# Performance work log

Measured on AMD Instinct MI355X. Metric: run time of the kernel, lower is better.

The kernel has to match this reference:

```python
import jax, jax.numpy as jnp
import numpy as np

NUM_HEADS = 16
PROJECT_DIM = 1024
HEAD_DIM = PROJECT_DIM // NUM_HEADS  # 64; used only for the softmax scale


def setup_inputs() -> dict:
    key = jax.random.key(0)
    k1, k2, k3 = jax.random.split(key, 3)
    B, N, D = 8, 3072, PROJECT_DIM
    inputs = jax.random.normal(k1, (B, N, D), dtype=jnp.float32)
    wqkv = jax.random.normal(k2, (D, 3 * D), dtype=jnp.float32) * (1.0 / np.sqrt(D))
    dense_w = jax.random.normal(k3, (3 * D, D), dtype=jnp.float32) * (1.0 / np.sqrt(3 * D))
    dense_b = jnp.zeros((D,), dtype=jnp.float32)
    return {"inputs": inputs, "wqkv": wqkv, "dense_w": dense_w, "dense_b": dense_b}


def reference(inputs, wqkv, dense_w, dense_b):
    B, N, D = inputs.shape
    H = NUM_HEADS
    # fused QKV projection: [B, N, 3D]
    qkv = jnp.einsum('bnd,de->bne', inputs, wqkv)
    # separate heads: [B, H, N, 3*head_dim]
    qkv = qkv.reshape(B, N, H, (3 * D) // H).transpose(0, 2, 1, 3)
    # NOTE: faithful to source — split along TOKEN axis (axis=2) into 3 chunks
    q, k, v = jnp.split(qkv, 3, axis=2)  # each [B, H, N//3, 3*head_dim]
    scale = 1.0 / jnp.sqrt(jnp.float32(HEAD_DIM))
    logits = jnp.einsum('bhqc,bhkc->bhqk', q, k) * scale  # [B, H, N//3, N//3]
    attn = jax.nn.softmax(logits, axis=-1)
    out = jnp.einsum('bhqk,bhkc->bhqc', attn, v)  # [B, H, N//3, 3*head_dim]
    # recombine heads -> [B, N//3, 3D]
    out = out.transpose(0, 2, 1, 3).reshape(B, N // 3, 3 * D)
    # output projection -> [B, N//3, D]
    return jnp.einsum('bnc,cd->bnd', out, dense_w) + dense_b
```

## Files before the change

kernel.cpp:

```cpp
#include <hip/hip_runtime.h>
#include <hip/hip_bf16.h>

typedef unsigned short u16;
using f32x4  = __attribute__((ext_vector_type(4))) float;
using bf16x8 = __attribute__((ext_vector_type(8))) short;

typedef __attribute__((address_space(1))) const void global_cvoid;
typedef __attribute__((address_space(3))) void lds_void;

__device__ __forceinline__ void async16(const u16* g, u16* l) {
    __builtin_amdgcn_global_load_lds((global_cvoid*)g, (lds_void*)l, 16, 0, 0);
}

__device__ __forceinline__ u16 f2bf(float f) {
    union { float f; unsigned u; } cv; cv.f = f;
    unsigned r = cv.u + 0x7fff + ((cv.u >> 16) & 1);
    return (u16)(r >> 16);
}

__device__ __forceinline__ u16 f2bf_rz(float f) {
    union { float f; unsigned u; } cv; cv.f = f;
    return (u16)(cv.u >> 16);
}

__device__ __forceinline__ float dppmax16(float x) {
    union { float f; int i; } c, o;
    c.f = x;
    o.i = __builtin_amdgcn_update_dpp(0, c.i, 0xB1,  0xF, 0xF, true); c.f = fmaxf(c.f, o.f);
    o.i = __builtin_amdgcn_update_dpp(0, c.i, 0x4E,  0xF, 0xF, true); c.f = fmaxf(c.f, o.f);
    o.i = __builtin_amdgcn_update_dpp(0, c.i, 0x141, 0xF, 0xF, true); c.f = fmaxf(c.f, o.f);
    o.i = __builtin_amdgcn_update_dpp(0, c.i, 0x140, 0xF, 0xF, true); c.f = fmaxf(c.f, o.f);
    return c.f;
}
__device__ __forceinline__ float dppsum16(float x) {
    union { float f; int i; } c, o;
    c.f = x;
    o.i = __builtin_amdgcn_update_dpp(0, c.i, 0xB1,  0xF, 0xF, true); c.f += o.f;
    o.i = __builtin_amdgcn_update_dpp(0, c.i, 0x4E,  0xF, 0xF, true); c.f += o.f;
    o.i = __builtin_amdgcn_update_dpp(0, c.i, 0x141, 0xF, 0xF, true); c.f += o.f;
    o.i = __builtin_amdgcn_update_dpp(0, c.i, 0x140, 0xF, 0xF, true); c.f += o.f;
    return c.f;
}

__global__ __launch_bounds__(256) void cast_kernel(const float* __restrict__ src,
                                                   u16* __restrict__ dst, int n4) {
    int i = blockIdx.x * blockDim.x + threadIdx.x;
    int st = gridDim.x * blockDim.x;
    for (; i < n4; i += st) {
        float4 v = ((const float4*)src)[i];
        ushort4 o;
        o.x = f2bf(v.x); o.y = f2bf(v.y); o.z = f2bf(v.z); o.w = f2bf(v.w);
        ((ushort4*)dst)[i] = o;
    }
}

__global__ __launch_bounds__(256) void wtrans_kernel(const float* __restrict__ src,
                                                     u16* __restrict__ dst, int R, int C) {
    __shared__ float tile[64][68];
    int ct = blockIdx.x, rt = blockIdx.y;
    int t = threadIdx.x;
    int r = t >> 2;
    const float* s = src + (size_t)(rt * 64 + r) * C + ct * 64;
#pragma unroll
    for (int jj = 0; jj < 4; ++jj) {
        int c4 = (t & 3) + jj * 4;
        float4 v = *(const float4*)(s + c4 * 4);
        *(float4*)&tile[r][c4 * 4] = v;
    }
    __syncthreads();
    int od = t >> 2;
    u16* d = dst + (size_t)(ct * 64 + od) * R + rt * 64;
#pragma unroll
    for (int jj = 0; jj < 4; ++jj) {
        int c4 = (t & 3) + jj * 4;
        ushort4 v;
        v.x = f2bf(tile[c4 * 4 + 0][od]);
        v.y = f2bf(tile[c4 * 4 + 1][od]);
        v.z = f2bf(tile[c4 * 4 + 2][od]);
        v.w = f2bf(tile[c4 * 4 + 3][od]);
        *(ushort4*)(d + c4 * 4) = v;
    }
}

template<bool OUT_F32>
__global__ __launch_bounds__(256, 2)
void gemm_bt_kernel(const u16* __restrict__ A, const u16* __restrict__ BT,
                    void* __restrict__ Cout, const float* __restrict__ bias,
                    u16* __restrict__ VTout,
                    int M, int N, int K) {
    __shared__ u16 lA[128 * 64];
    __shared__ u16 lB[128 * 64];
    const int t = threadIdx.x;
    const int w = t >> 6, lane = t & 63;
    const int nbx = N >> 7;
    const int nwg = gridDim.x;
    int bid = blockIdx.x;
    int cpx = nwg >> 3;
    int swz = (bid & 7) * cpx + (bid >> 3);
    const int bx = swz % nbx;
    const int by = swz / nbx;
    const size_t m0 = (size_t)by * 128, n0 = (size_t)bx * 128;

    const int lr = lane >> 3;
    const int lc = (lane & 7) * 8;
    const int wr = (w >> 1) * 64, wc = (w & 1) * 64;

    f32x4 acc[4][4] = {};

    for (int kk = 0; kk < K; kk += 64) {
        __syncthreads();
#pragma unroll
        for (int i = 0; i < 4; ++i) {
            int rr = (w * 4 + i) * 8 + lr;
            async16(A  + (m0 + rr) * (size_t)K + kk + lc, &lA[(w * 4 + i) * 512]);
            async16(BT + (n0 + rr) * (size_t)K + kk + lc, &lB[(w * 4 + i) * 512]);
        }
        __syncthreads();
#pragma unroll
        for (int ks = 0; ks < 2; ++ks) {
            bf16x8 af[4], bfv[4];
#pragma unroll
            for (int m = 0; m < 4; ++m)
                af[m] = *(const bf16x8*)&lA[(wr + m * 16 + (lane & 15)) * 64 + ks * 32 + (lane >> 4) * 8];
#pragma unroll
            for (int n = 0; n < 4; ++n)
                bfv[n] = *(const bf16x8*)&lB[(wc + n * 16 + (lane & 15)) * 64 + ks * 32 + (lane >> 4) * 8];
#pragma unroll
            for (int m = 0; m < 4; ++m)
#pragma unroll
                for (int n = 0; n < 4; ++n)
                    acc[m][n] = __builtin_amdgcn_mfma_f32_16x16x32_bf16(af[m], bfv[n], acc[m][n], 0, 0, 0);
        }
    }

    const int r0 = (lane >> 4) * 4;
    const int cl = lane & 15;
    if constexpr (OUT_F32) {
        float* C = (float*)Cout;
#pragma unroll
        for (int m = 0; m < 4; ++m) {
            size_t row = m0 + wr + m * 16 + r0;
#pragma unroll
            for (int n = 0; n < 4; ++n) {
                size_t col = n0 + wc + n * 16 + cl;
                float bv = bias[col];
#pragma unroll
                for (int r = 0; r < 4; ++r)
                    C[(row + r) * (size_t)N + col] = acc[m][n][r] + bv;
            }
        }
    } else {
        u16* C = (u16*)Cout;
#pragma unroll
        for (int m = 0; m < 4; ++m) {
            size_t row = m0 + wr + m * 16 + r0;
#pragma unroll
            for (int n = 0; n < 4; ++n) {
                size_t col = n0 + wc + n * 16 + cl;
#pragma unroll
                for (int r = 0; r < 4; ++r)
                    C[(row + r) * (size_t)N + col] = f2bf(acc[m][n][r]);
            }
        }
    }
}

__global__ __launch_bounds__(512, 2)
void gemm256_kernel(const u16* __restrict__ A, const u16* __restrict__ BT,
                    u16* __restrict__ Cout, u16* __restrict__ VTout,
                    int M, int N, int K) {
    __shared__ u16 lds[65536];
    u16* lA = lds;
    u16* lB = lds + 32768;

    const int t = threadIdx.x, w = t >> 6, l = t & 63;
    const int g = l >> 4, ql = l & 15;
    const int wm = w >> 2, wn = w & 3;
    const int nbx = N >> 8;
    int bid = blockIdx.x;
    int cpx = gridDim.x >> 3;
    int swz = (bid & 7) * cpx + (bid >> 3);
    const int bx = swz % nbx, by = swz / nbx;
    const size_t m0 = (size_t)by * 256, n0 = (size_t)bx * 256;

    const u16* Ag = A  + m0 * (size_t)K;
    const u16* Bg = BT + n0 * (size_t)K;

    unsigned soff[2];
#pragma unroll
    for (int i = 0; i < 2; ++i) {
        int ch = i * 512 + t;
        int r = ch >> 2, c = ch & 3;
        soff[i] = (unsigned)(r * K + (c ^ ((r >> 1) & 3)) * 8);
    }

#define STAGE8(kh3) do {                                                           \
    int sl_ = (kh3) & 3;                                                           \
    _Pragma("unroll")                                                              \
    for (int i = 0; i < 2; ++i) {                                                  \
        async16(Ag + soff[i] + (unsigned)(kh3) * 32u, lA + sl_ * 8192 + (i * 512 + w * 64) * 8); \
        async16(Bg + soff[i] + (unsigned)(kh3) * 32u, lB + sl_ * 8192 + (i * 512 + w * 64) * 8); \
    } } while (0)

    STAGE8(0); STAGE8(1); STAGE8(2);

    f32x4 acc[8][4] = {};
    const int cswz = (g ^ ((ql >> 1) & 3)) * 8;
    const int arow = wm * 128 + ql;
    const int brow = wn * 64 + ql;

    auto phase = [&](int kh, int vm, bool st) {
        if (vm == 8)      asm volatile("s_waitcnt vmcnt(8)" ::: "memory");
        else if (vm == 4) asm volatile("s_waitcnt vmcnt(4)" ::: "memory");
        else              asm volatile("s_waitcnt vmcnt(0)" ::: "memory");
        __builtin_amdgcn_s_barrier();
        const u16* sA = lA + (kh & 3) * 8192;
        const u16* sB = lB + (kh & 3) * 8192;
        bf16x8 fa[8], fb[4];
#pragma unroll
        for (int m = 0; m < 8; ++m)
            fa[m] = *(const bf16x8*)&sA[(arow + m * 16) * 32 + cswz];
#pragma unroll
        for (int n = 0; n < 4; ++n)
            fb[n] = *(const bf16x8*)&sB[(brow + n * 16) * 32 + cswz];
        if (st) STAGE8(kh + 3);
        __builtin_amdgcn_s_setprio(1);
#pragma unroll
        for (int m = 0; m < 8; ++m)
#pragma unroll
            for (int n = 0; n < 4; ++n)
                acc[m][n] = __builtin_amdgcn_mfma_f32_16x16x32_bf16(fa[m], fb[n], acc[m][n], 0, 0, 0);
        __builtin_amdgcn_s_setprio(0);
    };

    const int KH = K >> 5;
#pragma unroll 1
    for (int kh = 0; kh < KH - 3; ++kh) phase(kh, 8, true);
    phase(KH - 3, 8, false);
    phase(KH - 2, 4, false);
    phase(KH - 1, 0, false);

    const int r0 = g * 4;
    int tok0 = (int)(m0 % 3072);
    if (tok0 >= 2048) {
        int b = (int)(m0 / 3072);
#pragma unroll
        for (int m = 0; m < 8; ++m) {
            int tok = tok0 - 2048 + wm * 128 + m * 16 + r0;
#pragma unroll
            for (int n = 0; n < 4; ++n) {
                int col = (int)n0 + wn * 64 + n * 16 + ql;
                int h = col / 192, ch = col % 192;
                ushort4 v;
                v.x = f2bf(acc[m][n][0]);
                v.y = f2bf(acc[m][n][1]);
                v.z = f2bf(acc[m][n][2]);
                v.w = f2bf(acc[m][n][3]);
                *(ushort4*)(VTout + ((size_t)(b * 16 + h) * 192 + ch) * 1024 + tok) = v;
            }
        }
    } else {
        float qs = (tok0 < 1024) ? 0.1803368801111f : 1.0f;
#pragma unroll
        for (int m = 0; m < 8; ++m) {
            size_t row = m0 + wm * 128 + m * 16 + r0;
#pragma unroll
            for (int n = 0; n < 4; ++n) {
                size_t col = n0 + wn * 64 + n * 16 + ql;
#pragma unroll
                for (int r = 0; r < 4; ++r)
                    Cout[(row + r) * (size_t)N + col] = f2bf(acc[m][n][r] * qs);
            }
        }
    }
#undef STAGE8
}

__global__ __launch_bounds__(256, 2)
void attn_kernel(const u16* __restrict__ QKV, const u16* __restrict__ VT,
                 u16* __restrict__ comb) {
    __shared__ u16 lds[40960];
    u16* lK = lds;
    u16* lV = lds + 18432;
    u16* lP = lds + 36864;

    const int t = threadIdx.x, w = t >> 6, lane = t & 63;
    const int g = lane >> 4, ql = lane & 15;
    const int bid = blockIdx.x;
    const int gid = (bid & 7) * 128 + (bid >> 3);
    const int bh = gid >> 3, qt = gid & 7;
    const int b = bh >> 4, h = bh & 15;

    const u16* Qg  = QKV + ((size_t)(b * 3072 + qt * 128 + w * 32)) * 3072 + h * 192;
    const u16* Kg  = QKV + ((size_t)(b * 3072 + 1024)) * 3072 + h * 192;
    const u16* VTg = VT + (size_t)bh * 192 * 1024;

    unsigned koff[3], voff[3];
#pragma unroll
    for (int i = 0; i < 3; ++i) {
        int ch = i * 256 + t;
        int kr = ch / 24, kc = ch % 24;
        koff[i] = kr * 3072 + (kc ^ (kr & 7)) * 8;
        int vr = ch >> 2, vc = ch & 3;
        voff[i] = vr * 1024 + (vc ^ (vr & 3)) * 8;
    }

#define STAGE_KV(kt) do {                                                         \
    int sl_ = (kt) % 3;                                                           \
    _Pragma("unroll")                                                             \
    for (int i = 0; i < 3; ++i) {                                                 \
        async16(Kg + koff[i] + (unsigned)(kt) * 98304u, lK + sl_ * 6144 + (i * 256 + w * 64) * 8); \
        async16(VTg + voff[i] + (unsigned)(kt) * 32u,   lV + sl_ * 6144 + (i * 256 + w * 64) * 8); \
    } } while (0)

    STAGE_KV(0);
    STAGE_KV(1);

    bf16x8 aq[2][6];
#pragma unroll
    for (int rg = 0; rg < 2; ++rg)
#pragma unroll
        for (int cs = 0; cs < 6; ++cs)
            aq[rg][cs] = *(const bf16x8*)(Qg + (size_t)(rg * 16 + ql) * 3072
                                             + cs * 32 + g * 8);

    f32x4 acc_o[2][12] = {};
    float m2[2][4], lsum[2][4];
#pragma unroll
    for (int rg = 0; rg < 2; ++rg)
#pragma unroll
        for (int r = 0; r < 4; ++r) { m2[rg][r] = -1e30f; lsum[rg][r] = 0.f; }
    u16* lPw = &lP[w * 1024];
    const int pswz = (ql >> 2) & 3;

#pragma unroll 1
    for (int it = 0; it < 32; ++it) {
        if (it != 31) asm volatile("s_waitcnt vmcnt(6)" ::: "memory");
        else          asm volatile("s_waitcnt vmcnt(0)" ::: "memory");
        __builtin_amdgcn_s_barrier();
        if (it < 30) STAGE_KV(it + 2);

        const u16* sK = lK + (it % 3) * 6144;
        const u16* sV = lV + (it % 3) * 6144;

        f32x4 s[2][2] = {};
        __builtin_amdgcn_s_setprio(1);
#pragma unroll
        for (int kf = 0; kf < 2; ++kf) {
            const int krow = kf * 16 + ql;
#pragma unroll
            for (int cs = 0; cs < 6; ++cs) {
                bf16x8 bk = *(const bf16x8*)&sK[krow * 192 + ((cs * 4 + g) ^ (krow & 7)) * 8];
                s[0][kf] = __builtin_amdgcn_mfma_f32_16x16x32_bf16(aq[0][cs], bk, s[0][kf], 0, 0, 0);
                s[1][kf] = __builtin_amdgcn_mfma_f32_16x16x32_bf16(aq[1][cs], bk, s[1][kf], 0, 0, 0);
            }
        }
        __builtin_amdgcn_s_setprio(0);

#pragma unroll
        for (int rg = 0; rg < 2; ++rg) {
            float mx[4];
            bool need = false;
#pragma unroll
            for (int r = 0; r < 4; ++r) {
                float m = fmaxf(s[rg][0][r], s[rg][1][r]);
                mx[r] = dppmax16(m);
                need = need || (mx[r] > m2[rg][r] + 8.f);
            }
            if (__any((int)need)) {
#pragma unroll
                for (int r = 0; r < 4; ++r) {
                    float mn = fmaxf(m2[rg][r], mx[r]);
                    float fac = exp2f(m2[rg][r] - mn);
                    m2[rg][r] = mn;
                    lsum[rg][r] *= fac;
#pragma unroll
                    for (int df = 0; df < 12; ++df) acc_o[rg][df][r] *= fac;
                }
            }
#pragma unroll
            for (int r = 0; r < 4; ++r) {
                int q = rg * 16 + g * 4 + r;
                float rs = 0.f;
#pragma unroll
                for (int kf = 0; kf < 2; ++kf) {
                    float p = exp2f(s[rg][kf][r] - m2[rg][r]);
                    rs += p;
                    lPw[q * 32 + ((kf * 16 + ql) ^ (g << 3))] = f2bf_rz(p);
                }
                lsum[rg][r] += dppsum16(rs);
            }
        }

        __builtin_amdgcn_s_setprio(1);
        {
            bf16x8 pa0 = *(const bf16x8*)&lPw[ql * 32 + ((g ^ pswz) << 3)];
            bf16x8 pa1 = *(const bf16x8*)&lPw[(16 + ql) * 32 + ((g ^ pswz) << 3)];
#pragma unroll
            for (int df = 0; df < 12; ++df) {
                const int vrow = df * 16 + ql;
                bf16x8 bv = *(const bf16x8*)&sV[vrow * 32 + ((g ^ (vrow & 3)) << 3)];
                acc_o[0][df] = __builtin_amdgcn_mfma_f32_16x16x32_bf16(pa0, bv, acc_o[0][df], 0, 0, 0);
                acc_o[1][df] = __builtin_amdgcn_mfma_f32_16x16x32_bf16(pa1, bv, acc_o[1][df], 0, 0, 0);
            }
        }
        __builtin_amdgcn_s_setprio(0);
    }

    u16* dst = comb + ((size_t)(b * 1024 + qt * 128 + w * 32)) * 3072 + h * 192;
#pragma unroll
    for (int rg = 0; rg < 2; ++rg)
#pragma unroll
        for (int r = 0; r < 4; ++r) {
            int q = rg * 16 + g * 4 + r;
            float invl = 1.0f / lsum[rg][r];
#pragma unroll
            for (int df = 0; df < 12; ++df)
                dst[(size_t)q * 3072 + df * 16 + ql] = f2bf(acc_o[rg][df][r] * invl);
        }
#undef STAGE_KV
}

extern "C" void kernel_launch(void* const* d_in, const int* in_sizes, int n_in,
                              void* d_out, int out_size, void* d_ws, size_t ws_size,
                              hipStream_t stream) {
    const float* X  = (const float*)d_in[0];
    const float* W1 = (const float*)d_in[1];
    const float* W2 = (const float*)d_in[2];
    const float* Bb = (const float*)d_in[3];

    char* ws = (char*)d_ws;
    u16* Xb   = (u16*)(ws);
    u16* W1bT = (u16*)(ws + 50331648);
    u16* W2bT = (u16*)(ws + 56623104);
    u16* QKVb = (u16*)(ws + 62914560);
    u16* VT   = (u16*)(ws + 213909504);
    u16* comb = Xb;

    cast_kernel<<<2048, 256, 0, stream>>>(X, Xb, (8 * 3072 * 1024) / 4);
    wtrans_kernel<<<dim3(3072 / 64, 1024 / 64), 256, 0, stream>>>(W1, W1bT, 1024, 3072);
    wtrans_kernel<<<dim3(1024 / 64, 3072 / 64), 256, 0, stream>>>(W2, W2bT, 3072, 1024);
    gemm256_kernel<<<(24576 / 256) * (3072 / 256), 512, 0, stream>>>(
        Xb, W1bT, QKVb, VT, 24576, 3072, 1024);
    attn_kernel<<<1024, 256, 0, stream>>>(QKVb, VT, comb);
    gemm_bt_kernel<true><<<(8192 / 128) * (1024 / 128), 256, 0, stream>>>(
        comb, W2bT, d_out, Bb, nullptr, 8192, 1024, 3072);
}
```

Before: 420.1 us.

## Compute softmax row sums via MFMA with ones vector and share one max per row group

Drops the per-row DPP sum reduction and instead accumulates softmax denominators with an extra MFMA that multiplies the bf16 P tile by a vector of ones. It also replaces the per-row running maxima with a single maximum shared by each 16-row group, which shortens the max and rescale logic. The V tile swizzle in LDS is changed from (row&3) to ((row>>1)&3) to reduce bank conflicts. Side effects: the denominators now sum the bf16-truncated P values, and a shared group max could underflow rows whose logits sit far below the group maximum.

```diff
diff --git a/kernel.cpp b/kernel.cpp
--- a/kernel.cpp
+++ b/kernel.cpp
@@ -30,15 +30,6 @@
     o.i = __builtin_amdgcn_update_dpp(0, c.i, 0x4E,  0xF, 0xF, true); c.f = fmaxf(c.f, o.f);
     o.i = __builtin_amdgcn_update_dpp(0, c.i, 0x141, 0xF, 0xF, true); c.f = fmaxf(c.f, o.f);
     o.i = __builtin_amdgcn_update_dpp(0, c.i, 0x140, 0xF, 0xF, true); c.f = fmaxf(c.f, o.f);
-    return c.f;
-}
-__device__ __forceinline__ float dppsum16(float x) {
-    union { float f; int i; } c, o;
-    c.f = x;
-    o.i = __builtin_amdgcn_update_dpp(0, c.i, 0xB1,  0xF, 0xF, true); c.f += o.f;
-    o.i = __builtin_amdgcn_update_dpp(0, c.i, 0x4E,  0xF, 0xF, true); c.f += o.f;
-    o.i = __builtin_amdgcn_update_dpp(0, c.i, 0x141, 0xF, 0xF, true); c.f += o.f;
-    o.i = __builtin_amdgcn_update_dpp(0, c.i, 0x140, 0xF, 0xF, true); c.f += o.f;
     return c.f;
 }
 
@@ -302,7 +293,7 @@
         int kr = ch / 24, kc = ch % 24;
         koff[i] = kr * 3072 + (kc ^ (kr & 7)) * 8;
         int vr = ch >> 2, vc = ch & 3;
-        voff[i] = vr * 1024 + (vc ^ (vr & 3)) * 8;
+        voff[i] = vr * 1024 + (vc ^ ((vr >> 1) & 3)) * 8;
     }
 
 #define STAGE_KV(kt) do {                                                         \
@@ -324,12 +315,13 @@
             aq[rg][cs] = *(const bf16x8*)(Qg + (size_t)(rg * 16 + ql) * 3072
                                              + cs * 32 + g * 8);
 
+    bf16x8 vone;
+#pragma unroll
+    for (int j = 0; j < 8; ++j) vone[j] = (short)0x3F80;
+
     f32x4 acc_o[2][12] = {};
-    float m2[2][4], lsum[2][4];
-#pragma unroll
-    for (int rg = 0; rg < 2; ++rg)
-#pragma unroll
-        for (int r = 0; r < 4; ++r) { m2[rg][r] = -1e30f; lsum[rg][r] = 0.f; }
+    f32x4 acc_l[2] = {};
+    float m2[2] = {-1e30f, -1e30f};
     u16* lPw = &lP[w * 1024];
     const int pswz = (ql >> 2) & 3;
 
@@ -359,36 +351,29 @@
 
 #pragma unroll
         for (int rg = 0; rg < 2; ++rg) {
-            float mx[4];
-            bool need = false;
-#pragma unroll
-            for (int r = 0; r < 4; ++r) {
-                float m = fmaxf(s[rg][0][r], s[rg][1][r]);
-                mx[r] = dppmax16(m);
-                need = need || (mx[r] > m2[rg][r] + 8.f);
-            }
+            float m = s[rg][0][0];
+#pragma unroll
+            for (int kf = 0; kf < 2; ++kf)
+#pragma unroll
+                for (int r = 0; r < 4; ++r) m = fmaxf(m, s[rg][kf][r]);
+            float mx = dppmax16(m);
+            bool need = mx > m2[rg] + 8.f;
             if (__any((int)need)) {
-#pragma unroll
-                for (int r = 0; r < 4; ++r) {
-                    float mn = fmaxf(m2[rg][r], mx[r]);
-                    float fac = exp2f(m2[rg][r] - mn);
-                    m2[rg][r] = mn;
-                    lsum[rg][r] *= fac;
-#pragma unroll
-                    for (int df = 0; df < 12; ++df) acc_o[rg][df][r] *= fac;
-                }
+                float mn = fmaxf(m2[rg], mx);
+                float fac = exp2f(m2[rg] - mn);
+                m2[rg] = mn;
+                acc_l[rg] *= fac;
+#pragma unroll
+                for (int df = 0; df < 12; ++df) acc_o[rg][df] *= fac;
             }
 #pragma unroll
             for (int r = 0; r < 4; ++r) {
                 int q = rg * 16 + g * 4 + r;
-                float rs = 0.f;
 #pragma unroll
                 for (int kf = 0; kf < 2; ++kf) {
-                    float p = exp2f(s[rg][kf][r] - m2[rg][r]);
-                    rs += p;
+                    float p = exp2f(s[rg][kf][r] - m2[rg]);
                     lPw[q * 32 + ((kf * 16 + ql) ^ (g << 3))] = f2bf_rz(p);
                 }
-                lsum[rg][r] += dppsum16(rs);
             }
         }
 
@@ -396,10 +381,12 @@
         {
             bf16x8 pa0 = *(const bf16x8*)&lPw[ql * 32 + ((g ^ pswz) << 3)];
             bf16x8 pa1 = *(const bf16x8*)&lPw[(16 + ql) * 32 + ((g ^ pswz) << 3)];
+            acc_l[0] = __builtin_amdgcn_mfma_f32_16x16x32_bf16(pa0, vone, acc_l[0], 0, 0, 0);
+            acc_l[1] = __builtin_amdgcn_mfma_f32_16x16x32_bf16(pa1, vone, acc_l[1], 0, 0, 0);
 #pragma unroll
             for (int df = 0; df < 12; ++df) {
                 const int vrow = df * 16 + ql;
-                bf16x8 bv = *(const bf16x8*)&sV[vrow * 32 + ((g ^ (vrow & 3)) << 3)];
+                bf16x8 bv = *(const bf16x8*)&sV[vrow * 32 + ((g ^ ((vrow >> 1) & 3)) << 3)];
                 acc_o[0][df] = __builtin_amdgcn_mfma_f32_16x16x32_bf16(pa0, bv, acc_o[0][df], 0, 0, 0);
                 acc_o[1][df] = __builtin_amdgcn_mfma_f32_16x16x32_bf16(pa1, bv, acc_o[1][df], 0, 0, 0);
             }
@@ -413,7 +400,7 @@
 #pragma unroll
         for (int r = 0; r < 4; ++r) {
             int q = rg * 16 + g * 4 + r;
-            float invl = 1.0f / lsum[rg][r];
+            float invl = 1.0f / acc_l[rg][r];
 #pragma unroll
             for (int df = 0; df < 12; ++df)
                 dst[(size_t)q * 3072 + df * 16 + ql] = f2bf(acc_o[rg][df][r] * invl);
```

Result: faster. 386.7 us (median of 4 runs) (-7.9%).
